# Performance work log

Measured on AMD Instinct MI355X. Metric: run time of the kernel, lower is better.

The kernel has to match this reference:

```python
import jax, jax.numpy as jnp
import numpy as np

D_MODEL = 1024
NUM_HEADS = 16
HEAD_DIM = D_MODEL // NUM_HEADS


def setup_inputs() -> dict:
    key = jax.random.key(0)
    ks = jax.random.split(key, 10)
    B, SQ, SK = 2, 2048, 2048
    scale = 1.0 / np.sqrt(D_MODEL)
    inp = {
        "x1": jax.random.normal(ks[0], (B, SQ, D_MODEL), jnp.float32),
        "x2": jax.random.normal(ks[1], (B, SK, D_MODEL), jnp.float32),
        "Wq": jax.random.normal(ks[2], (D_MODEL, D_MODEL), jnp.float32) * scale,
        "bq": jnp.zeros((D_MODEL,), jnp.float32),
        "Wk": jax.random.normal(ks[3], (D_MODEL, D_MODEL), jnp.float32) * scale,
        "bk": jnp.zeros((D_MODEL,), jnp.float32),
        "Wv": jax.random.normal(ks[4], (D_MODEL, D_MODEL), jnp.float32) * scale,
        "bv": jnp.zeros((D_MODEL,), jnp.float32),
        "Wo": jax.random.normal(ks[5], (D_MODEL, D_MODEL), jnp.float32) * scale,
        "bo": jnp.zeros((D_MODEL,), jnp.float32),
    }
    return inp


def reference(x1, x2, Wq, bq, Wk, bk, Wv, bv, Wo, bo):
    B, SQ, _ = x1.shape
    SK = x2.shape[1]
    # projections, then split into heads: [B, H, S, Dh]
    def split_heads(t, S):
        return t.reshape(B, S, NUM_HEADS, HEAD_DIM).transpose(0, 2, 1, 3)
    Q = split_heads(x1 @ Wq + bq, SQ)
    K = split_heads(x2 @ Wk + bk, SK)
    V = split_heads(x2 @ Wv + bv, SK)
    # note: original scales by 1/head_dim**0.5
    scores = jnp.einsum("bhqd,bhkd->bhqk", Q, K) / jnp.sqrt(
        jnp.asarray(HEAD_DIM, Q.dtype))
    attn = jax.nn.softmax(scores, axis=-1)
    ctx = jnp.einsum("bhqk,bhkd->bhqd", attn, V)
    ctx = ctx.transpose(0, 2, 1, 3).reshape(B, SQ, D_MODEL)
    return ctx @ Wo + bo
```

## Files before the change

kernel.cpp:

```cpp
#include <hip/hip_runtime.h>
#include <stdint.h>


typedef unsigned short u16b;
typedef __attribute__((ext_vector_type(4))) short short4v;
typedef __attribute__((ext_vector_type(8))) short short8v;
typedef __attribute__((ext_vector_type(4))) float float4v;
typedef __attribute__((ext_vector_type(2))) unsigned int uint2v;

#if __has_builtin(__builtin_amdgcn_exp2f)
__device__ __forceinline__ float exp2_fast(float x){ return __builtin_amdgcn_exp2f(x); }
#else
__device__ __forceinline__ float exp2_fast(float x){ return exp2f(x); }
#endif

__device__ __forceinline__ float bf2f(u16b u) {
  union { unsigned int i; float f; } v; v.i = ((unsigned int)u) << 16; return v.f;
}
__device__ __forceinline__ u16b f2bf(float f) {
  union { float f; unsigned int i; } v; v.f = f;
  return (u16b)((v.i + 0x7fffu + ((v.i >> 16) & 1u)) >> 16);
}
__device__ __forceinline__ void gl_lds16(const u16b* g, u16b* l) {
  __builtin_amdgcn_global_load_lds(
      (const __attribute__((address_space(1))) void*)g,
      (__attribute__((address_space(3))) void*)l, 16, 0, 0);
}

__global__ __launch_bounds__(256) void cvt2_bf16(
    const float* __restrict__ s0, const float* __restrict__ s1,
    u16b* __restrict__ d0, u16b* __restrict__ d1, int n4) {
  const float* src = blockIdx.y ? s1 : s0;
  u16b* dst = blockIdx.y ? d1 : d0;
  int i = blockIdx.x * blockDim.x + threadIdx.x;
  int stride = gridDim.x * blockDim.x;
  for (; i < n4; i += stride) {
    float4v v = ((const float4v*)src)[i];
    short4v o;
    o[0]=(short)f2bf(v[0]); o[1]=(short)f2bf(v[1]);
    o[2]=(short)f2bf(v[2]); o[3]=(short)f2bf(v[3]);
    ((short4v*)dst)[i] = o;
  }
}

__global__ __launch_bounds__(256) void transposeW(
    const float* __restrict__ W0, const float* __restrict__ W1,
    const float* __restrict__ W2, const float* __restrict__ W3,
    u16b* __restrict__ out) {
  __shared__ u16b tile[32][33];
  const int z = blockIdx.z;
  const float* src = (z==0) ? W0 : (z==1) ? W1 : (z==2) ? W2 : W3;
  u16b* dst = out + (size_t)z * (1024*1024);
  const int x = threadIdx.x, y = threadIdx.y;
  const int bx = blockIdx.x * 32, by = blockIdx.y * 32;
#pragma unroll
  for (int j=0;j<4;++j)
    tile[y*4+j][x] = f2bf(src[(size_t)(by + y*4+j)*1024 + bx + x]);
  __syncthreads();
#pragma unroll
  for (int j=0;j<4;++j)
    dst[(size_t)(bx + y*4+j)*1024 + by + x] = tile[x][y*4+j];
}

template<int BN, bool OUT_F32, bool BIAS_ROW>
__device__ __forceinline__ void gemm_core(
    u16b* __restrict__ As, u16b* __restrict__ Bs,
    const u16b* __restrict__ A, const u16b* __restrict__ Bt,
    const float* __restrict__ bias, void* __restrict__ Cv,
    int N, int K, int bm, int bn) {
  constexpr int NT = BN / 32;
  const int tid = threadIdx.x;
  const int lane = tid & 63, wave = tid >> 6;
  const int wm = wave >> 1, wn = wave & 1;
  const int l15 = lane & 15, l4 = lane >> 4;
  float4v acc[4][NT];
#pragma unroll
  for (int i=0;i<4;++i)
#pragma unroll
    for (int j=0;j<NT;++j) acc[i][j] = (float4v){0.f,0.f,0.f,0.f};

  const int swz = (l15 >> 1) & 3;

  for (int k0 = 0; k0 < K; k0 += 32) {
    __syncthreads();
    {
      int row = tid >> 2, seg = tid & 3;
      int segg0 = seg ^ ((row >> 1) & 3);
      int row2 = row + 64;
      int segg1 = seg ^ ((row2 >> 1) & 3);
      gl_lds16(&A[(size_t)(bm+row )*K + k0 + segg0*8], &As[tid*8]);
      gl_lds16(&A[(size_t)(bm+row2)*K + k0 + segg1*8], &As[(tid+256)*8]);
      gl_lds16(&Bt[(size_t)(bn+row )*K + k0 + segg0*8], &Bs[tid*8]);
      if (BN == 128)
        gl_lds16(&Bt[(size_t)(bn+row2)*K + k0 + segg1*8], &Bs[(tid+256)*8]);
    }
    __syncthreads();
    short8v af[4], bf[NT];
#pragma unroll
    for (int mt=0;mt<4;++mt)
      af[mt] = *(const short8v*)&As[(wm*64+mt*16+l15)*32 + ((l4 ^ swz)*8)];
#pragma unroll
    for (int nt=0;nt<NT;++nt)
      bf[nt] = *(const short8v*)&Bs[(wn*(BN/2)+nt*16+l15)*32 + ((l4 ^ swz)*8)];
#pragma unroll
    for (int mt=0;mt<4;++mt)
#pragma unroll
      for (int nt=0;nt<NT;++nt)
        acc[mt][nt] = __builtin_amdgcn_mfma_f32_16x16x32_bf16(af[mt], bf[nt], acc[mt][nt], 0, 0, 0);
  }

#pragma unroll
  for (int nt=0;nt<NT;++nt) {
    int col = bn + wn*(BN/2) + nt*16 + l15;
    float bbc = BIAS_ROW ? 0.f : bias[col];
#pragma unroll
    for (int mt=0;mt<4;++mt) {
      int row0 = bm + wm*64 + mt*16 + l4*4;
#pragma unroll
      for (int r=0;r<4;++r) {
        float bb = BIAS_ROW ? bias[row0+r] : bbc;
        float v = acc[mt][nt][r] + bb;
        if (OUT_F32) ((float*)Cv)[(size_t)(row0+r)*N + col] = v;
        else         ((u16b*)Cv)[(size_t)(row0+r)*N + col] = f2bf(v);
      }
    }
  }
}

__global__ __launch_bounds__(256) void gemm_qkv(
    const u16b* __restrict__ x1b, const u16b* __restrict__ x2b,
    const u16b* __restrict__ WT, const float* __restrict__ bq,
    const float* __restrict__ bk, const float* __restrict__ bv,
    u16b* __restrict__ QKV) {
  __shared__ __align__(16) u16b As[128*32];
  __shared__ __align__(16) u16b Bs[128*32];
  const int z = blockIdx.z;
  const size_t Mi = 1024*1024;
  if (z == 2) {
    gemm_core<128,false,true>(As, Bs, WT + 2*Mi, x2b, bv, QKV + 8*Mi,
                              4096, 1024, blockIdx.x*128, blockIdx.y*128);
  } else {
    gemm_core<128,false,false>(As, Bs, z ? x2b : x1b, WT + (size_t)z*Mi,
                               z ? bk : bq, QKV + (size_t)z*4*Mi,
                               1024, 1024, blockIdx.y*128, blockIdx.x*128);
  }
}

__global__ __launch_bounds__(256) void gemm_out(
    const u16b* __restrict__ A, const u16b* __restrict__ Bt,
    const float* __restrict__ bias, float* __restrict__ C) {
  __shared__ __align__(16) u16b As[128*32];
  __shared__ __align__(16) u16b Bs[64*32];
  gemm_core<64,true,false>(As, Bs, A, Bt, bias, C, 1024, 1024,
                           blockIdx.y*128, blockIdx.x*64);
}

__global__ __launch_bounds__(256) void attn_q64(
    const u16b* __restrict__ Q, const u16b* __restrict__ Kg,
    const u16b* __restrict__ Vt, u16b* __restrict__ O) {
  __shared__ __align__(16) u16b Ks[128*64];
  __shared__ __align__(16) u16b Vs[64*128];
  __shared__ __align__(16) u16b Ps[4*16*64];
  const int tid = threadIdx.x;
  const int lane = tid & 63, wave = tid >> 6;
  const int l15 = lane & 15, l4 = lane >> 4;
  const int bh = blockIdx.x;
  const int b = bh >> 4, h = bh & 15;
  const int q0 = blockIdx.y * 64;
  const size_t seqbase = (size_t)b * 2048;
  const int colh = h * 64;
  u16b* Pw = Ps + wave * 1024;

  const float qscale = 0.125f * 1.4426950408889634f;
  short8v qf[2];
  {
    size_t qrow = seqbase + q0 + wave*16 + l15;
#pragma unroll
    for (int ks=0; ks<2; ++ks) {
      short8v raw = *(const short8v*)&Q[qrow*1024 + colh + ks*32 + l4*8];
      short8v s;
#pragma unroll
      for (int i=0;i<8;++i) s[i] = (short)f2bf(bf2f((u16b)raw[i]) * qscale);
      qf[ks] = s;
    }
  }

  short8v ones;
#pragma unroll
  for (int i=0;i<8;++i) ones[i] = (short)0x3F80;

  float4v lacc = (float4v){0.f,0.f,0.f,0.f};
  float4v oacc[4];
#pragma unroll
  for (int nb=0; nb<4; ++nb) oacc[nb] = (float4v){0.f,0.f,0.f,0.f};

  for (int kt = 0; kt < 16; ++kt) {
    const size_t kvbase = seqbase + (size_t)kt*128;
    __syncthreads();
#pragma unroll
    for (int j=0; j<4; ++j) {
      int idx = j*256 + tid;
      {
        int row = idx >> 3, seg = idx & 7;
        gl_lds16(&Kg[(kvbase+row)*1024 + colh + ((seg ^ (row & 7))*8)], &Ks[idx*8]);
      }
      {
        int row = idx >> 4, seg = idx & 15;
        gl_lds16(&Vt[(size_t)(h*64+row)*4096 + (size_t)b*2048 + kt*128
                     + ((seg ^ (row & 15))*8)], &Vs[idx*8]);
      }
    }
    __syncthreads();

    float4v sacc[8];
#pragma unroll
    for (int nb=0; nb<8; ++nb) sacc[nb] = (float4v){0.f,0.f,0.f,0.f};
#pragma unroll
    for (int nb=0; nb<8; ++nb)
#pragma unroll
      for (int ks=0; ks<2; ++ks) {
        short8v kf = *(const short8v*)&Ks[(nb*16+l15)*64 + (((ks*4+l4) ^ (l15 & 7))*8)];
        sacc[nb] = __builtin_amdgcn_mfma_f32_16x16x32_bf16(kf, qf[ks], sacc[nb], 0, 0, 0);
      }

#pragma unroll
    for (int h2=0; h2<2; ++h2) {
#pragma unroll
      for (int nbl=0; nbl<4; ++nbl) {
        const float4v s4 = sacc[h2*4 + nbl];
        unsigned int u0 = __float_as_uint(exp2_fast(s4[0]));
        unsigned int u1 = __float_as_uint(exp2_fast(s4[1]));
        unsigned int u2 = __float_as_uint(exp2_fast(s4[2]));
        unsigned int u3 = __float_as_uint(exp2_fast(s4[3]));
        uint2v dw;
        dw[0] = (u0 >> 16) | (u1 & 0xFFFF0000u);
        dw[1] = (u2 >> 16) | (u3 & 0xFFFF0000u);
        *(uint2v*)&Pw[l15*64 + (((nbl*4 + l4) ^ l15)*4)] = dw;
      }
      __asm__ __volatile__("s_waitcnt lgkmcnt(0)" ::: "memory");

#pragma unroll
      for (int ks2=0; ks2<2; ++ks2) {
        int c0 = (ks2*8 + l4*2) ^ l15;
        int c1 = (ks2*8 + l4*2 + 1) ^ l15;
        short4v pa = *(const short4v*)&Pw[l15*64 + c0*4];
        short4v pb = *(const short4v*)&Pw[l15*64 + c1*4];
        short8v pf;
        pf[0]=pa[0]; pf[1]=pa[1]; pf[2]=pa[2]; pf[3]=pa[3];
        pf[4]=pb[0]; pf[5]=pb[1]; pf[6]=pb[2]; pf[7]=pb[3];
        lacc = __builtin_amdgcn_mfma_f32_16x16x32_bf16(pf, ones, lacc, 0, 0, 0);
#pragma unroll
        for (int nb=0; nb<4; ++nb) {
          int cc = (h2*8 + ks2*4 + l4) ^ l15;
          short8v vf = *(const short8v*)&Vs[(nb*16+l15)*128 + cc*8];
          oacc[nb] = __builtin_amdgcn_mfma_f32_16x16x32_bf16(pf, vf, oacc[nb], 0, 0, 0);
        }
      }
    }
  }

#pragma unroll
  for (int r=0; r<4; ++r) {
    float inv = 1.0f / lacc[r];
    size_t row = seqbase + q0 + wave*16 + l4*4 + r;
#pragma unroll
    for (int nb=0; nb<4; ++nb)
      O[row*1024 + colh + nb*16 + l15] = f2bf(oacc[nb][r] * inv);
  }
}

extern "C" void kernel_launch(void* const* d_in, const int* in_sizes, int n_in,
                              void* d_out, int out_size, void* d_ws, size_t ws_size,
                              hipStream_t stream) {
  const float* x1 = (const float*)d_in[0];
  const float* x2 = (const float*)d_in[1];
  const float* Wq = (const float*)d_in[2];
  const float* bq = (const float*)d_in[3];
  const float* Wk = (const float*)d_in[4];
  const float* bk = (const float*)d_in[5];
  const float* Wv = (const float*)d_in[6];
  const float* bv = (const float*)d_in[7];
  const float* Wo = (const float*)d_in[8];
  const float* bo = (const float*)d_in[9];
  (void)in_sizes; (void)n_in; (void)out_size; (void)ws_size;

  u16b* ws = (u16b*)d_ws;
  const size_t Mi = 1024*1024;
  u16b* WT  = ws;
  u16b* WoT = ws + 3*Mi;
  u16b* x1b = ws + 4*Mi;
  u16b* x2b = ws + 8*Mi;
  u16b* QKV = ws + 12*Mi;
  u16b* Qb  = QKV;
  u16b* Kb  = QKV + 4*Mi;
  u16b* Vtb = QKV + 8*Mi;
  u16b* Cx  = x1b;

  cvt2_bf16<<<dim3(1024,2), 256, 0, stream>>>(x1, x2, x1b, x2b, (int)Mi);
  transposeW<<<dim3(32,32,4), dim3(32,8,1), 0, stream>>>(Wq, Wk, Wv, Wo, WT);

  gemm_qkv<<<dim3(8,32,3), 256, 0, stream>>>(x1b, x2b, WT, bq, bk, bv, QKV);

  attn_q64<<<dim3(32,32), 256, 0, stream>>>(Qb, Kb, Vtb, Cx);

  gemm_out<<<dim3(16,32), 256, 0, stream>>>(Cx, WoT, bo, (float*)d_out);
}
```

Baseline: 227.7 us.

## Double attention query tile, fold Q scaling into GEMM, merge prep kernels

The attention kernel now handles 128 query rows per block, with two 16-row groups per wave, so each K/V tile loaded into LDS serves twice as many queries and global K/V traffic is halved. The softmax scale and log2e factor are applied in the QKV GEMM epilogue for Q, which removes the per-element rescale from attention. The bf16 conversion and weight transpose kernels are merged into one launch. In exchange, the attention kernel uses more registers and has half as many blocks, and Q is now rounded to bf16 after scaling instead of before.

```diff
diff --git a/kernel.cpp b/kernel.cpp
--- a/kernel.cpp
+++ b/kernel.cpp
@@ -14,9 +14,6 @@
 __device__ __forceinline__ float exp2_fast(float x){ return exp2f(x); }
 #endif
 
-__device__ __forceinline__ float bf2f(u16b u) {
-  union { unsigned int i; float f; } v; v.i = ((unsigned int)u) << 16; return v.f;
-}
 __device__ __forceinline__ u16b f2bf(float f) {
   union { float f; unsigned int i; } v; v.f = f;
   return (u16b)((v.i + 0x7fffu + ((v.i >> 16) & 1u)) >> 16);
@@ -27,39 +24,41 @@
       (__attribute__((address_space(3))) void*)l, 16, 0, 0);
 }
 
-__global__ __launch_bounds__(256) void cvt2_bf16(
-    const float* __restrict__ s0, const float* __restrict__ s1,
-    u16b* __restrict__ d0, u16b* __restrict__ d1, int n4) {
-  const float* src = blockIdx.y ? s1 : s0;
-  u16b* dst = blockIdx.y ? d1 : d0;
-  int i = blockIdx.x * blockDim.x + threadIdx.x;
-  int stride = gridDim.x * blockDim.x;
-  for (; i < n4; i += stride) {
-    float4v v = ((const float4v*)src)[i];
-    short4v o;
-    o[0]=(short)f2bf(v[0]); o[1]=(short)f2bf(v[1]);
-    o[2]=(short)f2bf(v[2]); o[3]=(short)f2bf(v[3]);
-    ((short4v*)dst)[i] = o;
-  }
-}
-
-__global__ __launch_bounds__(256) void transposeW(
+__global__ __launch_bounds__(256) void prep(
+    const float* __restrict__ x1, const float* __restrict__ x2,
     const float* __restrict__ W0, const float* __restrict__ W1,
     const float* __restrict__ W2, const float* __restrict__ W3,
-    u16b* __restrict__ out) {
-  __shared__ u16b tile[32][33];
-  const int z = blockIdx.z;
-  const float* src = (z==0) ? W0 : (z==1) ? W1 : (z==2) ? W2 : W3;
-  u16b* dst = out + (size_t)z * (1024*1024);
-  const int x = threadIdx.x, y = threadIdx.y;
-  const int bx = blockIdx.x * 32, by = blockIdx.y * 32;
-#pragma unroll
-  for (int j=0;j<4;++j)
-    tile[y*4+j][x] = f2bf(src[(size_t)(by + y*4+j)*1024 + bx + x]);
-  __syncthreads();
-#pragma unroll
-  for (int j=0;j<4;++j)
-    dst[(size_t)(bx + y*4+j)*1024 + by + x] = tile[x][y*4+j];
+    u16b* __restrict__ x1b, u16b* __restrict__ x2b, u16b* __restrict__ WT) {
+  const int tid = threadIdx.x;
+  const int mode = blockIdx.y;
+  if (mode < 2) {
+    const float* src = mode ? x2 : x1;
+    u16b* dst = mode ? x2b : x1b;
+    const int n4 = 1024*1024;
+    int i = blockIdx.x * 256 + tid;
+    const int stride = gridDim.x * 256;
+    for (; i < n4; i += stride) {
+      float4v v = ((const float4v*)src)[i];
+      short4v o;
+      o[0]=(short)f2bf(v[0]); o[1]=(short)f2bf(v[1]);
+      o[2]=(short)f2bf(v[2]); o[3]=(short)f2bf(v[3]);
+      ((short4v*)dst)[i] = o;
+    }
+  } else {
+    __shared__ u16b tile[32][33];
+    const int z = mode - 2;
+    const float* src = (z==0) ? W0 : (z==1) ? W1 : (z==2) ? W2 : W3;
+    u16b* dst = WT + (size_t)z * (1024*1024);
+    const int x = tid & 31, y = tid >> 5;
+    const int bx = (blockIdx.x & 31) * 32, by = (blockIdx.x >> 5) * 32;
+#pragma unroll
+    for (int j=0;j<4;++j)
+      tile[y*4+j][x] = f2bf(src[(size_t)(by + y*4+j)*1024 + bx + x]);
+    __syncthreads();
+#pragma unroll
+    for (int j=0;j<4;++j)
+      dst[(size_t)(bx + y*4+j)*1024 + by + x] = tile[x][y*4+j];
+  }
 }
 
 template<int BN, bool OUT_F32, bool BIAS_ROW>
@@ -67,7 +66,7 @@
     u16b* __restrict__ As, u16b* __restrict__ Bs,
     const u16b* __restrict__ A, const u16b* __restrict__ Bt,
     const float* __restrict__ bias, void* __restrict__ Cv,
-    int N, int K, int bm, int bn) {
+    int N, int K, int bm, int bn, float oscale) {
   constexpr int NT = BN / 32;
   const int tid = threadIdx.x;
   const int lane = tid & 63, wave = tid >> 6;
@@ -119,7 +118,7 @@
 #pragma unroll
       for (int r=0;r<4;++r) {
         float bb = BIAS_ROW ? bias[row0+r] : bbc;
-        float v = acc[mt][nt][r] + bb;
+        float v = (acc[mt][nt][r] + bb) * oscale;
         if (OUT_F32) ((float*)Cv)[(size_t)(row0+r)*N + col] = v;
         else         ((u16b*)Cv)[(size_t)(row0+r)*N + col] = f2bf(v);
       }
@@ -136,13 +135,15 @@
   __shared__ __align__(16) u16b Bs[128*32];
   const int z = blockIdx.z;
   const size_t Mi = 1024*1024;
+  const float QSCALE = 0.125f * 1.4426950408889634f;
   if (z == 2) {
     gemm_core<128,false,true>(As, Bs, WT + 2*Mi, x2b, bv, QKV + 8*Mi,
-                              4096, 1024, blockIdx.x*128, blockIdx.y*128);
+                              4096, 1024, blockIdx.x*128, blockIdx.y*128, 1.0f);
   } else {
     gemm_core<128,false,false>(As, Bs, z ? x2b : x1b, WT + (size_t)z*Mi,
                                z ? bk : bq, QKV + (size_t)z*4*Mi,
-                               1024, 1024, blockIdx.y*128, blockIdx.x*128);
+                               1024, 1024, blockIdx.y*128, blockIdx.x*128,
+                               z ? 1.0f : QSCALE);
   }
 }
 
@@ -152,47 +153,44 @@
   __shared__ __align__(16) u16b As[128*32];
   __shared__ __align__(16) u16b Bs[64*32];
   gemm_core<64,true,false>(As, Bs, A, Bt, bias, C, 1024, 1024,
-                           blockIdx.y*128, blockIdx.x*64);
-}
-
-__global__ __launch_bounds__(256) void attn_q64(
+                           blockIdx.y*128, blockIdx.x*64, 1.0f);
+}
+
+__global__ __launch_bounds__(256, 2) void attn_q128(
     const u16b* __restrict__ Q, const u16b* __restrict__ Kg,
     const u16b* __restrict__ Vt, u16b* __restrict__ O) {
   __shared__ __align__(16) u16b Ks[128*64];
   __shared__ __align__(16) u16b Vs[64*128];
-  __shared__ __align__(16) u16b Ps[4*16*64];
+  __shared__ __align__(16) u16b Ps[4*2*1024];
   const int tid = threadIdx.x;
   const int lane = tid & 63, wave = tid >> 6;
   const int l15 = lane & 15, l4 = lane >> 4;
   const int bh = blockIdx.x;
   const int b = bh >> 4, h = bh & 15;
-  const int q0 = blockIdx.y * 64;
+  const int q0 = blockIdx.y * 128;
   const size_t seqbase = (size_t)b * 2048;
   const int colh = h * 64;
-  u16b* Pw = Ps + wave * 1024;
-
-  const float qscale = 0.125f * 1.4426950408889634f;
-  short8v qf[2];
-  {
-    size_t qrow = seqbase + q0 + wave*16 + l15;
-#pragma unroll
-    for (int ks=0; ks<2; ++ks) {
-      short8v raw = *(const short8v*)&Q[qrow*1024 + colh + ks*32 + l4*8];
-      short8v s;
-#pragma unroll
-      for (int i=0;i<8;++i) s[i] = (short)f2bf(bf2f((u16b)raw[i]) * qscale);
-      qf[ks] = s;
-    }
+  u16b* Pw = Ps + wave * 2048;
+
+  short8v qf[2][2];
+#pragma unroll
+  for (int g=0; g<2; ++g) {
+    size_t qrow = seqbase + q0 + wave*32 + g*16 + l15;
+#pragma unroll
+    for (int ks=0; ks<2; ++ks)
+      qf[g][ks] = *(const short8v*)&Q[qrow*1024 + colh + ks*32 + l4*8];
   }
 
   short8v ones;
 #pragma unroll
   for (int i=0;i<8;++i) ones[i] = (short)0x3F80;
 
-  float4v lacc = (float4v){0.f,0.f,0.f,0.f};
-  float4v oacc[4];
-#pragma unroll
-  for (int nb=0; nb<4; ++nb) oacc[nb] = (float4v){0.f,0.f,0.f,0.f};
+  float4v lacc[2] = {(float4v){0.f,0.f,0.f,0.f}, (float4v){0.f,0.f,0.f,0.f}};
+  float4v oacc[2][4];
+#pragma unroll
+  for (int g=0; g<2; ++g)
+#pragma unroll
+    for (int nb=0; nb<4; ++nb) oacc[g][nb] = (float4v){0.f,0.f,0.f,0.f};
 
   for (int kt = 0; kt < 16; ++kt) {
     const size_t kvbase = seqbase + (size_t)kt*128;
@@ -212,61 +210,74 @@
     }
     __syncthreads();
 
-    float4v sacc[8];
-#pragma unroll
-    for (int nb=0; nb<8; ++nb) sacc[nb] = (float4v){0.f,0.f,0.f,0.f};
+    float4v sacc[2][8];
+#pragma unroll
+    for (int g=0; g<2; ++g)
+#pragma unroll
+      for (int nb=0; nb<8; ++nb) sacc[g][nb] = (float4v){0.f,0.f,0.f,0.f};
 #pragma unroll
     for (int nb=0; nb<8; ++nb)
 #pragma unroll
       for (int ks=0; ks<2; ++ks) {
         short8v kf = *(const short8v*)&Ks[(nb*16+l15)*64 + (((ks*4+l4) ^ (l15 & 7))*8)];
-        sacc[nb] = __builtin_amdgcn_mfma_f32_16x16x32_bf16(kf, qf[ks], sacc[nb], 0, 0, 0);
+        sacc[0][nb] = __builtin_amdgcn_mfma_f32_16x16x32_bf16(kf, qf[0][ks], sacc[0][nb], 0, 0, 0);
+        sacc[1][nb] = __builtin_amdgcn_mfma_f32_16x16x32_bf16(kf, qf[1][ks], sacc[1][nb], 0, 0, 0);
       }
 
 #pragma unroll
     for (int h2=0; h2<2; ++h2) {
 #pragma unroll
-      for (int nbl=0; nbl<4; ++nbl) {
-        const float4v s4 = sacc[h2*4 + nbl];
-        unsigned int u0 = __float_as_uint(exp2_fast(s4[0]));
-        unsigned int u1 = __float_as_uint(exp2_fast(s4[1]));
-        unsigned int u2 = __float_as_uint(exp2_fast(s4[2]));
-        unsigned int u3 = __float_as_uint(exp2_fast(s4[3]));
-        uint2v dw;
-        dw[0] = (u0 >> 16) | (u1 & 0xFFFF0000u);
-        dw[1] = (u2 >> 16) | (u3 & 0xFFFF0000u);
-        *(uint2v*)&Pw[l15*64 + (((nbl*4 + l4) ^ l15)*4)] = dw;
-      }
+      for (int g=0; g<2; ++g)
+#pragma unroll
+        for (int nbl=0; nbl<4; ++nbl) {
+          const float4v s4 = sacc[g][h2*4 + nbl];
+          unsigned int u0 = __float_as_uint(exp2_fast(s4[0]));
+          unsigned int u1 = __float_as_uint(exp2_fast(s4[1]));
+          unsigned int u2 = __float_as_uint(exp2_fast(s4[2]));
+          unsigned int u3 = __float_as_uint(exp2_fast(s4[3]));
+          uint2v dw;
+          dw[0] = (u0 >> 16) | (u1 & 0xFFFF0000u);
+          dw[1] = (u2 >> 16) | (u3 & 0xFFFF0000u);
+          *(uint2v*)&Pw[g*1024 + l15*64 + (((nbl*4 + l4) ^ l15)*4)] = dw;
+        }
       __asm__ __volatile__("s_waitcnt lgkmcnt(0)" ::: "memory");
 
 #pragma unroll
       for (int ks2=0; ks2<2; ++ks2) {
-        int c0 = (ks2*8 + l4*2) ^ l15;
-        int c1 = (ks2*8 + l4*2 + 1) ^ l15;
-        short4v pa = *(const short4v*)&Pw[l15*64 + c0*4];
-        short4v pb = *(const short4v*)&Pw[l15*64 + c1*4];
-        short8v pf;
-        pf[0]=pa[0]; pf[1]=pa[1]; pf[2]=pa[2]; pf[3]=pa[3];
-        pf[4]=pb[0]; pf[5]=pb[1]; pf[6]=pb[2]; pf[7]=pb[3];
-        lacc = __builtin_amdgcn_mfma_f32_16x16x32_bf16(pf, ones, lacc, 0, 0, 0);
+        short8v pf[2];
+#pragma unroll
+        for (int g=0; g<2; ++g) {
+          int c0 = (ks2*8 + l4*2) ^ l15;
+          int c1 = (ks2*8 + l4*2 + 1) ^ l15;
+          short4v pa = *(const short4v*)&Pw[g*1024 + l15*64 + c0*4];
+          short4v pb = *(const short4v*)&Pw[g*1024 + l15*64 + c1*4];
+          short8v p;
+          p[0]=pa[0]; p[1]=pa[1]; p[2]=pa[2]; p[3]=pa[3];
+          p[4]=pb[0]; p[5]=pb[1]; p[6]=pb[2]; p[7]=pb[3];
+          pf[g] = p;
+          lacc[g] = __builtin_amdgcn_mfma_f32_16x16x32_bf16(p, ones, lacc[g], 0, 0, 0);
+        }
 #pragma unroll
         for (int nb=0; nb<4; ++nb) {
           int cc = (h2*8 + ks2*4 + l4) ^ l15;
           short8v vf = *(const short8v*)&Vs[(nb*16+l15)*128 + cc*8];
-          oacc[nb] = __builtin_amdgcn_mfma_f32_16x16x32_bf16(pf, vf, oacc[nb], 0, 0, 0);
+          oacc[0][nb] = __builtin_amdgcn_mfma_f32_16x16x32_bf16(pf[0], vf, oacc[0][nb], 0, 0, 0);
+          oacc[1][nb] = __builtin_amdgcn_mfma_f32_16x16x32_bf16(pf[1], vf, oacc[1][nb], 0, 0, 0);
         }
       }
     }
   }
 
 #pragma unroll
-  for (int r=0; r<4; ++r) {
-    float inv = 1.0f / lacc[r];
-    size_t row = seqbase + q0 + wave*16 + l4*4 + r;
-#pragma unroll
-    for (int nb=0; nb<4; ++nb)
-      O[row*1024 + colh + nb*16 + l15] = f2bf(oacc[nb][r] * inv);
-  }
+  for (int g=0; g<2; ++g)
+#pragma unroll
+    for (int r=0; r<4; ++r) {
+      float inv = 1.0f / lacc[g][r];
+      size_t row = seqbase + q0 + wave*32 + g*16 + l4*4 + r;
+#pragma unroll
+      for (int nb=0; nb<4; ++nb)
+        O[row*1024 + colh + nb*16 + l15] = f2bf(oacc[g][nb][r] * inv);
+    }
 }
 
 extern "C" void kernel_launch(void* const* d_in, const int* in_sizes, int n_in,
@@ -296,12 +307,11 @@
   u16b* Vtb = QKV + 8*Mi;
   u16b* Cx  = x1b;
 
-  cvt2_bf16<<<dim3(1024,2), 256, 0, stream>>>(x1, x2, x1b, x2b, (int)Mi);
-  transposeW<<<dim3(32,32,4), dim3(32,8,1), 0, stream>>>(Wq, Wk, Wv, Wo, WT);
+  prep<<<dim3(1024,6), 256, 0, stream>>>(x1, x2, Wq, Wk, Wv, Wo, x1b, x2b, WT);
 
   gemm_qkv<<<dim3(8,32,3), 256, 0, stream>>>(x1b, x2b, WT, bq, bk, bv, QKV);
 
-  attn_q64<<<dim3(32,32), 256, 0, stream>>>(Qb, Kb, Vtb, Cx);
+  attn_q128<<<dim3(32,16), 256, 0, stream>>>(Qb, Kb, Vtb, Cx);
 
   gemm_out<<<dim3(16,32), 256, 0, stream>>>(Cx, WoT, bo, (float*)d_out);
 }
```

New measurement: 216.8 us. -4.8%, faster.
